# Performance work log

Hardware: AMD Instinct MI355X
Metric: run time of the kernel (lower is better)

Reference implementation:

```python
import jax, jax.numpy as jnp
import numpy as np

HIDDEN = 2048
NH = 32       # num query heads
NKV = 8       # num kv heads
D = 64        # head_dim = hidden // NH
BSX, BSY = 32, 32  # block sizes


def setup_inputs() -> dict:
    key = jax.random.key(0)
    ks = jax.random.split(key, 5)
    B, L = 2, 4096  # L = x_dim * y_dim
    w = lambda k, sh, fan: jax.random.normal(k, sh, jnp.float32) * (fan ** -0.5)
    return {
        "hidden_states": jax.random.normal(ks[0], (B, L, HIDDEN), jnp.float32),
        "Wq": w(ks[1], (HIDDEN, NH * D), HIDDEN),
        "Wk": w(ks[2], (HIDDEN, NKV * D), HIDDEN),
        "Wv": w(ks[3], (HIDDEN, NKV * D), HIDDEN),
        "Wo": w(ks[4], (NH * D, HIDDEN), NH * D),
        "x_dim": 64,
        "y_dim": 64,
    }


def _block_split(x, B, bnx, bny, h):
    # einops: 'b (bnx bsx bny bsy) (h d) -> (b bnx bny) (bsx bsy) h d'
    x = x.reshape(B, bnx, BSX, bny, BSY, h, D)
    x = x.transpose(0, 1, 3, 2, 4, 5, 6)  # b bnx bny bsx bsy h d
    return x.reshape(B * bnx * bny, BSX * BSY, h, D)


def reference(hidden_states, Wq, Wk, Wv, Wo, x_dim, y_dim):
    B, L, _ = hidden_states.shape
    bnx, bny = x_dim // BSX, y_dim // BSY
    q = _block_split(hidden_states @ Wq, B, bnx, bny, NH)   # [nb, T, NH, D]
    k = _block_split(hidden_states @ Wk, B, bnx, bny, NKV)  # [nb, T, NKV, D]
    v = _block_split(hidden_states @ Wv, B, bnx, bny, NKV)
    g = NH // NKV  # GQA groups: query head i attends kv head i // g
    k = jnp.repeat(k, g, axis=2)
    v = jnp.repeat(v, g, axis=2)
    scores = jnp.einsum('nqhd,nkhd->nhqk', q, k) * (D ** -0.5)
    p = jax.nn.softmax(scores, axis=-1)
    o = jnp.einsum('nhqk,nkhd->nqhd', p, v)  # [nb, T, NH, D]
    # Faithful to the torch code: plain reshape (does NOT invert the block rearrange)
    o = o.reshape(B, L, NH * D)
    return o @ Wo
```

## Files before the change

### kernel.cpp

```cpp
#include <hip/hip_runtime.h>

typedef __bf16 bf16_t;
typedef __bf16 bf16x8 __attribute__((ext_vector_type(8)));
typedef __bf16 bf16x4 __attribute__((ext_vector_type(4)));
typedef float f32x4 __attribute__((ext_vector_type(4)));
typedef float f32x16 __attribute__((ext_vector_type(16)));
typedef short s16x4 __attribute__((ext_vector_type(4)));
typedef short s16x8 __attribute__((ext_vector_type(8)));

#define MFMA16(A_, B_, C_) __builtin_amdgcn_mfma_f32_16x16x32_bf16((A_), (B_), (C_), 0, 0, 0)
#define MFMA32(A_, B_, C_) __builtin_amdgcn_mfma_f32_32x32x16_bf16((A_), (B_), (C_), 0, 0, 0)

#define QSC 0.18033688011112042f

__device__ __forceinline__ void gload_lds16(const bf16_t* g, bf16_t* l) {
  __builtin_amdgcn_global_load_lds(
      (const __attribute__((address_space(1))) void*)g,
      (__attribute__((address_space(3))) void*)l, 16, 0, 0);
}

__device__ __forceinline__ unsigned cvt_pk_bf16(float a, float b) {
  unsigned r;
  asm("v_cvt_pk_bf16_f32 %0, %1, %2" : "=v"(r) : "v"(a), "v"(b));
  return r;
}

__device__ __forceinline__ s16x4 tr_b16(const bf16_t* p) {
  s16x4 d;
  unsigned off = (unsigned)(size_t)(const __attribute__((address_space(3))) bf16_t*)p;
  asm volatile("ds_read_b64_tr_b16 %0, %1" : "=v"(d) : "v"(off));
  return d;
}

union B128 { s16x8 s; bf16x8 b; };

#define DSR(PTR, U)                                                           \
  do {                                                                        \
    unsigned _o = (unsigned)(size_t)                                          \
        (const __attribute__((address_space(3))) bf16_t*)(PTR);               \
    asm volatile("ds_read_b128 %0, %1" : "=v"((U).s) : "v"(_o));              \
  } while (0)

__device__ __forceinline__ void swap32(unsigned a, unsigned b, int hi,
                                       unsigned& ra, unsigned& rb) {
  unsigned bx = (unsigned)__shfl_xor((int)b, 32);
  unsigned ax = (unsigned)__shfl_xor((int)a, 32);
  ra = hi ? a : bx;
  rb = hi ? ax : b;
}

__global__ __launch_bounds__(256) void k_convert(const float* __restrict__ in,
                                                 bf16_t* __restrict__ out, int n4) {
  int i = blockIdx.x * 256 + threadIdx.x;
  if (i >= n4) return;
  float4 v = ((const float4*)in)[i];
  bf16x4 o;
  o[0] = (__bf16)v.x; o[1] = (__bf16)v.y; o[2] = (__bf16)v.z; o[3] = (__bf16)v.w;
  *(bf16x4*)(out + (size_t)i * 4) = o;
}

__global__ __launch_bounds__(256) void k_transpose(const float* __restrict__ in,
                                                   bf16_t* __restrict__ out, int R, int C) {
  __shared__ float tile[64][65];
  int tx = threadIdx.x & 63;
  int ty = threadIdx.x >> 6;
  int bc = blockIdx.x * 64;
  int br = blockIdx.y * 64;
#pragma unroll
  for (int i = ty; i < 64; i += 4)
    tile[i][tx] = in[(size_t)(br + i) * C + bc + tx];
  __syncthreads();
#pragma unroll
  for (int i = ty; i < 64; i += 4)
    out[(size_t)(bc + i) * R + br + tx] = (bf16_t)tile[tx][i];
}

__device__ __forceinline__ int permrow(int r) {
  int b  = r >> 12;
  int l  = r & 4095;
  int ix = (l >> 11) & 1;
  int sx = (l >> 6) & 31;
  int iy = (l >> 5) & 1;
  int sy = l & 31;
  return (b << 12) + (ix << 11) + (iy << 10) + (sx << 5) + sy;
}

#define LSLOT(B_, M_, H_) (lds + (((B_)*4 + (M_)*2 + (H_)) << 13))

#define STAGE_A(BUF, HF, T)                                                     \
  gload_lds16(aB + (size_t)((HF)*128) * 2048 + (T)*64, LSLOT(BUF, 0, HF) + wofs); \
  gload_lds16(aB + (size_t)((HF)*128 + 64) * 2048 + (T)*64,                     \
              LSLOT(BUF, 0, HF) + wofs + 4096);

#define STAGE_B(BUF, HF, T)                                                     \
  gload_lds16(bB + (size_t)((HF)*128) * 2048 + (T)*64, LSLOT(BUF, 1, HF) + wofs); \
  gload_lds16(bB + (size_t)((HF)*128 + 64) * 2048 + (T)*64,                     \
              LSLOT(BUF, 1, HF) + wofs + 4096);

#define LOAD_A(BUF, Q)                                                          \
  { const bf16_t* Ah = LSLOT(BUF, 0, wm) + ((Q)*32 + cl) * 64;                  \
    DSR(Ah + ((g16 * 8) ^ swz8), af[0][0]);                                     \
    DSR(Ah + ((32 + g16 * 8) ^ swz8), af[0][1]);                                \
    DSR(Ah + 1024 + ((g16 * 8) ^ swz8), af[1][0]);                              \
    DSR(Ah + 1024 + ((32 + g16 * 8) ^ swz8), af[1][1]); }

#define LOAD_B(BUF)                                                             \
  { const bf16_t* Bh = LSLOT(BUF, 1, wn >> 1);                                  \
    _Pragma("unroll") for (int ni = 0; ni < 4; ++ni) {                          \
      const bf16_t* Br = Bh + ((wn & 1) * 64 + ni * 16 + cl) * 64;              \
      DSR(Br + ((g16 * 8) ^ swz8), bfr[ni][0]);                                 \
      DSR(Br + ((32 + g16 * 8) ^ swz8), bfr[ni][1]); } }

#define MFMA_QUAD(Q)                                                            \
  _Pragma("unroll") for (int kk = 0; kk < 2; ++kk)                              \
    _Pragma("unroll") for (int ni = 0; ni < 4; ++ni) {                          \
      acc[2*(Q)][ni]   = MFMA16(af[0][kk].b, bfr[ni][kk].b, acc[2*(Q)][ni]);    \
      acc[2*(Q)+1][ni] = MFMA16(af[1][kk].b, bfr[ni][kk].b, acc[2*(Q)+1][ni]); }

#define PH_MID(VM4)                                                             \
  if (VM4) asm volatile("s_waitcnt vmcnt(4)" ::: "memory");                     \
  __builtin_amdgcn_s_barrier();                                                 \
  asm volatile("s_waitcnt lgkmcnt(0)" ::: "memory");                            \
  __builtin_amdgcn_sched_barrier(0);                                            \
  __builtin_amdgcn_s_setprio(1);

#define PH_END                                                                  \
  __builtin_amdgcn_sched_barrier(0);                                            \
  __builtin_amdgcn_s_setprio(0);                                                \
  __builtin_amdgcn_s_barrier();

template <int MODE>
__global__ __launch_bounds__(512, 2) void k_gemm8(
    const bf16_t* __restrict__ A,
    const bf16_t* __restrict__ B0, const bf16_t* __restrict__ B1,
    const bf16_t* __restrict__ B2,
    bf16_t* __restrict__ Cq, bf16_t* __restrict__ Ck, bf16_t* __restrict__ Cv,
    float* __restrict__ Cf) {
  extern __shared__ bf16_t lds[];

  int nwg = gridDim.x;
  int cpx = nwg >> 3;
  int bid = blockIdx.x;
  int swz = (bid & 7) * cpx + (bid >> 3);
  int tm = swz & 31;
  int tn = swz >> 5;

  const bf16_t* Bp;
  int brow;
  if (MODE == 0) {
    if (tn < 8)       { Bp = B0; brow = tn << 8; }
    else if (tn < 10) { Bp = B1; brow = (tn - 8) << 8; }
    else              { Bp = B2; brow = (tn - 10) << 8; }
  } else {
    Bp = B0; brow = tn << 8;
  }

  int tid = threadIdx.x;
  int lane = tid & 63;
  int w = tid >> 6;
  int wm = w >> 2, wn = w & 3;
  int g16 = lane >> 4, cl = lane & 15;
  int swz8 = (cl & 7) << 3;
  int wofs = w << 9;

  int srow = tid >> 3;
  int lc = (((tid & 7) ^ (srow & 7)) << 3);
  const bf16_t* aB = A + (size_t)(tm * 256 + srow) * 2048 + lc;
  const bf16_t* bB = Bp + (size_t)(brow + srow) * 2048 + lc;

  f32x4 acc[8][4];
#pragma unroll
  for (int i = 0; i < 8; ++i)
#pragma unroll
    for (int j = 0; j < 4; ++j) acc[i][j] = (f32x4)(0.0f);

  STAGE_A(0, 0, 0); STAGE_A(0, 1, 0);
  STAGE_B(0, 0, 0); STAGE_B(0, 1, 0);
  STAGE_B(1, 0, 1); STAGE_B(1, 1, 1);
  asm volatile("s_waitcnt vmcnt(4)" ::: "memory");
  __builtin_amdgcn_s_barrier();

  for (int it2 = 0; it2 < 16; ++it2) {
    int t1 = 2 * it2 + 1;
    int tf = 2 * it2 + 2; if (tf > 31) tf = 31;
    int tg = 2 * it2 + 3; if (tg > 31) tg = 31;
    B128 af[2][2], bfr[4][2];
    STAGE_A(1, 0, t1);
    LOAD_B(0); LOAD_A(0, 0);
    PH_MID(0); MFMA_QUAD(0); PH_END;
    STAGE_A(1, 1, t1);
    LOAD_A(0, 1);
    PH_MID(0); MFMA_QUAD(1); PH_END;
    STAGE_B(0, 0, tf);
    LOAD_A(0, 2);
    PH_MID(0); MFMA_QUAD(2); PH_END;
    STAGE_B(0, 1, tf);
    LOAD_A(0, 3);
    PH_MID(1); MFMA_QUAD(3); PH_END;
    STAGE_A(0, 0, tf);
    LOAD_B(1); LOAD_A(1, 0);
    PH_MID(0); MFMA_QUAD(0); PH_END;
    STAGE_A(0, 1, tf);
    LOAD_A(1, 1);
    PH_MID(0); MFMA_QUAD(1); PH_END;
    STAGE_B(1, 0, tg);
    LOAD_A(1, 2);
    PH_MID(0); MFMA_QUAD(2); PH_END;
    STAGE_B(1, 1, tg);
    LOAD_A(1, 3);
    PH_MID(1); MFMA_QUAD(3); PH_END;
  }

#pragma unroll
  for (int mi = 0; mi < 8; ++mi) {
#pragma unroll
    for (int rr = 0; rr < 4; ++rr) {
      int r = tm * 256 + wm * 128 + mi * 16 + g16 * 4 + rr;
      if (MODE == 0) {
        int rp = permrow(r);
#pragma unroll
        for (int ni = 0; ni < 4; ++ni) {
          int c = tn * 256 + wn * 64 + ni * 16 + cl;
          float v = acc[mi][ni][rr];
          if (c < 2048)      Cq[(size_t)rp * 2048 + c] = (bf16_t)(v * QSC);
          else if (c < 2560) Ck[(size_t)rp * 512 + (c - 2048)] = (bf16_t)v;
          else               Cv[(size_t)rp * 512 + (c - 2560)] = (bf16_t)v;
        }
      } else {
#pragma unroll
        for (int ni = 0; ni < 4; ++ni) {
          int c = tn * 256 + wn * 64 + ni * 16 + cl;
          Cf[(size_t)r * 2048 + c] = acc[mi][ni][rr];
        }
      }
    }
  }
}

__global__ __launch_bounds__(256, 2) void k_attn(
    const bf16_t* __restrict__ Qp, const bf16_t* __restrict__ Kp,
    const bf16_t* __restrict__ Vp, bf16_t* __restrict__ O) {
  int bid = blockIdx.x;
  int qc = bid & 7;
  int h  = (bid >> 3) & 31;
  int n  = bid >> 8;
  int kvh = h >> 2;

  __shared__ bf16_t buf[2][8192];

  int tid = threadIdx.x, lane = tid & 63, w = tid >> 6;
  int l31 = lane & 31, hi = lane >> 5;
  int qrow_blk = n * 1024 + qc * 128;
  bf16_t* base = &buf[0][0];

#pragma unroll
  for (int r = 0; r < 4; ++r) {
    int ql = r * 32 + (tid >> 3);
    int cs = (tid & 7) << 4;
    int lc = (cs ^ ((ql & 7) << 4)) >> 1;
    gload_lds16(Qp + (size_t)(qrow_blk + ql) * 2048 + h * 64 + lc,
                base + r * 2048 + w * 512);
  }
  __syncthreads();
  bf16x8 qf[4];
  {
    int q = w * 32 + l31;
    const bf16_t* qrow = base + q * 64;
    int sw = (q & 7) << 4;
#pragma unroll
    for (int c = 0; c < 4; ++c)
      qf[c] = *(const bf16x8*)(qrow + (((c * 32 + hi * 16) ^ sw) >> 1));
  }
  __syncthreads();

  f32x16 oacc0 = (f32x16)(0.0f), oacc1 = (f32x16)(0.0f);
  float m_run = -1e30f, l_run = 0.0f;

  auto stageKV = [&](int t) {
    bf16_t* bp = &buf[t & 1][0];
    int kvb = n * 1024 + t * 64;
#pragma unroll
    for (int r = 0; r < 2; ++r) {
      int kv = r * 32 + (tid >> 3);
      int cs = (tid & 7) << 4;
      int lc = (cs ^ ((kv & 7) << 4)) >> 1;
      gload_lds16(Kp + (size_t)(kvb + kv) * 512 + kvh * 64 + lc,
                  bp + r * 2048 + w * 512);
    }
#pragma unroll
    for (int r = 0; r < 2; ++r) {
      int slot = r * 256 + tid;
      int sub = slot >> 3;
      int kb = sub >> 2, db = sub & 3;
      int j = (slot >> 1) & 3, hf = slot & 1;
      gload_lds16(Vp + (size_t)(kvb + kb * 4 + j) * 512 + kvh * 64 + db * 16 + hf * 8,
                  bp + 4096 + r * 2048 + w * 512);
    }
  };

  stageKV(0);
  for (int t = 0; t < 16; ++t) {
    __syncthreads();
    if (t < 15) stageKV(t + 1);
    const bf16_t* bp = &buf[t & 1][0];
    const bf16_t* Vs = bp + 4096;

#pragma unroll
    for (int s = 0; s < 2; ++s) {
      f32x16 st = (f32x16)(0.0f);
      {
        int kv = s * 32 + l31;
        const bf16_t* krow = bp + kv * 64;
        int sw = (kv & 7) << 4;
#pragma unroll
        for (int c = 0; c < 4; ++c) {
          bf16x8 kf = *(const bf16x8*)(krow + (((c * 32 + hi * 16) ^ sw) >> 1));
          st = MFMA32(kf, qf[c], st);
        }
      }
      float a0 = fmaxf(st[0], st[1]),   a1 = fmaxf(st[2], st[3]);
      float a2 = fmaxf(st[4], st[5]),   a3 = fmaxf(st[6], st[7]);
      float a4 = fmaxf(st[8], st[9]),   a5 = fmaxf(st[10], st[11]);
      float a6 = fmaxf(st[12], st[13]), a7 = fmaxf(st[14], st[15]);
      float pmax = fmaxf(fmaxf(fmaxf(a0, a1), fmaxf(a2, a3)),
                         fmaxf(fmaxf(a4, a5), fmaxf(a6, a7)));
      pmax = fmaxf(pmax, __shfl_xor(pmax, 32));
      if (!__all(pmax <= m_run + 11.0f)) {
        float mnew = fmaxf(m_run, pmax);
        float resc = exp2f(m_run - mnew);
        l_run *= resc;
#pragma unroll
        for (int e = 0; e < 16; ++e) { oacc0[e] *= resc; oacc1[e] *= resc; }
        m_run = mnew;
      }
      float rs = 0.0f;
      unsigned pw[8];
#pragma unroll
      for (int u = 0; u < 8; ++u) {
        float p0 = exp2f(st[2 * u] - m_run);
        float p1 = exp2f(st[2 * u + 1] - m_run);
        rs += p0 + p1;
        pw[u] = cvt_pk_bf16(p0, p1);
      }
      rs += __shfl_xor(rs, 32);
      l_run += rs;

#pragma unroll
      for (int c = 0; c < 2; ++c) {
        unsigned w2, w0, w3, w1;
        swap32(pw[c * 4 + 2], pw[c * 4 + 0], hi, w2, w0);
        swap32(pw[c * 4 + 3], pw[c * 4 + 1], hi, w3, w1);
        union { unsigned u[4]; bf16x8 v; } pa;
        pa.u[0] = w0; pa.u[1] = w1; pa.u[2] = w2; pa.u[3] = w3;
        int kb0 = s * 8 + c * 4 + hi * 2;
        int dbl = l31 >> 4;
        int cc8 = (l31 & 15) * 4;
        const bf16_t* p00 = Vs + (kb0 * 4 + dbl) * 64 + cc8;
        const bf16_t* p01 = Vs + ((kb0 + 1) * 4 + dbl) * 64 + cc8;
        const bf16_t* p10 = Vs + (kb0 * 4 + 2 + dbl) * 64 + cc8;
        const bf16_t* p11 = Vs + ((kb0 + 1) * 4 + 2 + dbl) * 64 + cc8;
        s16x4 t00 = tr_b16(p00), t01 = tr_b16(p01);
        s16x4 t10 = tr_b16(p10), t11 = tr_b16(p11);
        asm volatile("s_waitcnt lgkmcnt(0)" ::: "memory");
        __builtin_amdgcn_sched_barrier(0);
        union { s16x4 s4[2]; bf16x8 v; } vf0, vf1;
        vf0.s4[0] = t00; vf0.s4[1] = t01;
        vf1.s4[0] = t10; vf1.s4[1] = t11;
        oacc0 = MFMA32(pa.v, vf0.v, oacc0);
        oacc1 = MFMA32(pa.v, vf1.v, oacc1);
      }
    }
  }

  float linv = 1.0f / l_run;
#pragma unroll
  for (int r = 0; r < 16; ++r) {
    int qrw = (r & 3) + 8 * (r >> 2) + 4 * hi;
    float li = __shfl(linv, qrw);
    size_t orow = (size_t)(qrow_blk + w * 32 + qrw) * 2048 + h * 64 + l31;
    O[orow]      = (bf16_t)(oacc0[r] * li);
    O[orow + 32] = (bf16_t)(oacc1[r] * li);
  }
}

extern "C" void kernel_launch(void* const* d_in, const int* in_sizes, int n_in,
                              void* d_out, int out_size, void* d_ws, size_t ws_size,
                              hipStream_t stream) {
  const float* X  = (const float*)d_in[0];
  const float* Wq = (const float*)d_in[1];
  const float* Wk = (const float*)d_in[2];
  const float* Wv = (const float*)d_in[3];
  const float* Wo = (const float*)d_in[4];
  float* out = (float*)d_out;

  char* ws = (char*)d_ws;
  const size_t MB = 1024 * 1024;
  bf16_t* Xb  = (bf16_t*)(ws + 0);
  bf16_t* WqT = (bf16_t*)(ws + 32 * MB);
  bf16_t* WkT = (bf16_t*)(ws + 40 * MB);
  bf16_t* WvT = (bf16_t*)(ws + 42 * MB);
  bf16_t* WoT = (bf16_t*)(ws + 44 * MB);
  bf16_t* Qp  = (bf16_t*)(ws + 52 * MB);
  bf16_t* Kp  = (bf16_t*)(ws + 84 * MB);
  bf16_t* Vp  = (bf16_t*)(ws + 92 * MB);
  bf16_t* Ob  = (bf16_t*)(ws + 100 * MB);

  hipFuncSetAttribute(reinterpret_cast<const void*>(&k_gemm8<0>),
                      hipFuncAttributeMaxDynamicSharedMemorySize, 131072);
  hipFuncSetAttribute(reinterpret_cast<const void*>(&k_gemm8<1>),
                      hipFuncAttributeMaxDynamicSharedMemorySize, 131072);

  k_convert<<<16384, 256, 0, stream>>>(X, Xb, 4194304);
  k_transpose<<<dim3(32, 32), 256, 0, stream>>>(Wq, WqT, 2048, 2048);
  k_transpose<<<dim3(8, 32), 256, 0, stream>>>(Wk, WkT, 2048, 512);
  k_transpose<<<dim3(8, 32), 256, 0, stream>>>(Wv, WvT, 2048, 512);
  k_transpose<<<dim3(32, 32), 256, 0, stream>>>(Wo, WoT, 2048, 2048);

  k_gemm8<0><<<384, 512, 131072, stream>>>(Xb, WqT, WkT, WvT, Qp, Kp, Vp, nullptr);
  k_attn<<<2048, 256, 0, stream>>>(Qp, Kp, Vp, Ob);
  k_gemm8<1><<<256, 512, 131072, stream>>>(Ob, WoT, nullptr, nullptr, nullptr,
                                           nullptr, nullptr, out);
}
```

Measured before the change: 354.2 us.

## Merge GEMM pipeline phases into fewer, larger MFMA blocks and retile block swizzle

Restructures the 8-phase-per-iteration GEMM main loop into 4 phases. Each phase now loads four A fragments and issues 32 MFMAs instead of 16, which halves the number of barriers and priority switches per K-step. The workgroup-to-tile mapping is also changed so each XCD-group of blocks covers 4 consecutive M-tiles across all N-tiles, to improve L2 reuse. The cost is higher register pressure from the larger fragment arrays and coarser overlap between global staging and compute.

```diff
diff --git a/kernel.cpp b/kernel.cpp
--- a/kernel.cpp
+++ b/kernel.cpp
@@ -97,12 +97,11 @@
   gload_lds16(bB + (size_t)((HF)*128 + 64) * 2048 + (T)*64,                     \
               LSLOT(BUF, 1, HF) + wofs + 4096);
 
-#define LOAD_A(BUF, Q)                                                          \
-  { const bf16_t* Ah = LSLOT(BUF, 0, wm) + ((Q)*32 + cl) * 64;                  \
-    DSR(Ah + ((g16 * 8) ^ swz8), af[0][0]);                                     \
-    DSR(Ah + ((32 + g16 * 8) ^ swz8), af[0][1]);                                \
-    DSR(Ah + 1024 + ((g16 * 8) ^ swz8), af[1][0]);                              \
-    DSR(Ah + 1024 + ((32 + g16 * 8) ^ swz8), af[1][1]); }
+#define LOAD_A2(BUF, H)                                                         \
+  { const bf16_t* Ah = LSLOT(BUF, 0, wm) + ((H)*64 + cl) * 64;                  \
+    _Pragma("unroll") for (int j = 0; j < 4; ++j) {                             \
+      DSR(Ah + j * 1024 + ((g16 * 8) ^ swz8), af[j][0]);                        \
+      DSR(Ah + j * 1024 + ((32 + g16 * 8) ^ swz8), af[j][1]); } }
 
 #define LOAD_B(BUF)                                                             \
   { const bf16_t* Bh = LSLOT(BUF, 1, wn >> 1);                                  \
@@ -111,11 +110,12 @@
       DSR(Br + ((g16 * 8) ^ swz8), bfr[ni][0]);                                 \
       DSR(Br + ((32 + g16 * 8) ^ swz8), bfr[ni][1]); } }
 
-#define MFMA_QUAD(Q)                                                            \
+#define MFMA_OCT(H)                                                             \
   _Pragma("unroll") for (int kk = 0; kk < 2; ++kk)                              \
-    _Pragma("unroll") for (int ni = 0; ni < 4; ++ni) {                          \
-      acc[2*(Q)][ni]   = MFMA16(af[0][kk].b, bfr[ni][kk].b, acc[2*(Q)][ni]);    \
-      acc[2*(Q)+1][ni] = MFMA16(af[1][kk].b, bfr[ni][kk].b, acc[2*(Q)+1][ni]); }
+    _Pragma("unroll") for (int j = 0; j < 4; ++j)                               \
+      _Pragma("unroll") for (int ni = 0; ni < 4; ++ni)                          \
+        acc[(H)*4 + j][ni] =                                                    \
+            MFMA16(af[j][kk].b, bfr[ni][kk].b, acc[(H)*4 + j][ni]);
 
 #define PH_MID(VM4)                                                             \
   if (VM4) asm volatile("s_waitcnt vmcnt(4)" ::: "memory");                     \
@@ -138,12 +138,11 @@
     float* __restrict__ Cf) {
   extern __shared__ bf16_t lds[];
 
-  int nwg = gridDim.x;
-  int cpx = nwg >> 3;
+  const int TN = (MODE == 0) ? 12 : 8;
   int bid = blockIdx.x;
-  int swz = (bid & 7) * cpx + (bid >> 3);
-  int tm = swz & 31;
-  int tn = swz >> 5;
+  int s = bid >> 3;
+  int tm = (bid & 7) * 4 + s / TN;
+  int tn = s % TN;
 
   const bf16_t* Bp;
   int brow;
@@ -184,31 +183,19 @@
     int t1 = 2 * it2 + 1;
     int tf = 2 * it2 + 2; if (tf > 31) tf = 31;
     int tg = 2 * it2 + 3; if (tg > 31) tg = 31;
-    B128 af[2][2], bfr[4][2];
-    STAGE_A(1, 0, t1);
-    LOAD_B(0); LOAD_A(0, 0);
-    PH_MID(0); MFMA_QUAD(0); PH_END;
-    STAGE_A(1, 1, t1);
-    LOAD_A(0, 1);
-    PH_MID(0); MFMA_QUAD(1); PH_END;
-    STAGE_B(0, 0, tf);
-    LOAD_A(0, 2);
-    PH_MID(0); MFMA_QUAD(2); PH_END;
-    STAGE_B(0, 1, tf);
-    LOAD_A(0, 3);
-    PH_MID(1); MFMA_QUAD(3); PH_END;
-    STAGE_A(0, 0, tf);
-    LOAD_B(1); LOAD_A(1, 0);
-    PH_MID(0); MFMA_QUAD(0); PH_END;
-    STAGE_A(0, 1, tf);
-    LOAD_A(1, 1);
-    PH_MID(0); MFMA_QUAD(1); PH_END;
-    STAGE_B(1, 0, tg);
-    LOAD_A(1, 2);
-    PH_MID(0); MFMA_QUAD(2); PH_END;
-    STAGE_B(1, 1, tg);
-    LOAD_A(1, 3);
-    PH_MID(1); MFMA_QUAD(3); PH_END;
+    B128 af[4][2], bfr[4][2];
+    STAGE_A(1, 0, t1); STAGE_A(1, 1, t1);
+    LOAD_B(0); LOAD_A2(0, 0);
+    PH_MID(0); MFMA_OCT(0); PH_END;
+    STAGE_B(0, 0, tf); STAGE_B(0, 1, tf);
+    LOAD_A2(0, 1);
+    PH_MID(1); MFMA_OCT(1); PH_END;
+    STAGE_A(0, 0, tf); STAGE_A(0, 1, tf);
+    LOAD_B(1); LOAD_A2(1, 0);
+    PH_MID(0); MFMA_OCT(0); PH_END;
+    STAGE_B(1, 0, tg); STAGE_B(1, 1, tg);
+    LOAD_A2(1, 1);
+    PH_MID(1); MFMA_OCT(1); PH_END;
   }
 
 #pragma unroll
```

After: 354.7 us. No clear change (+0.1%).

## Use 256x128 tiles with triple-buffered LDS pipeline for QKV projection GEMM

Applied to the files above, without the earlier changes.

Replaces the templated 256x256-tile GEMM for the fused QKV projection with a dedicated kernel using 256x128 tiles, 768 workgroups, and a three-slot LDS ring buffer that stages two k-steps ahead. This raises the workgroup count so the 256 CUs are filled more evenly (384 large tiles leave a partial second wave). It also changes the block-to-tile mapping to a fixed XCD-aware swizzle for both GEMMs. The cost is lower arithmetic intensity per tile, so more global traffic for the shared operand, and 144KB of LDS per workgroup, which limits each CU to one resident workgroup.

```diff
diff --git a/kernel.cpp b/kernel.cpp
--- a/kernel.cpp
+++ b/kernel.cpp
@@ -85,6 +85,128 @@
   return (b << 12) + (ix << 11) + (iy << 10) + (sx << 5) + sy;
 }
 
+#define SBAR __builtin_amdgcn_sched_barrier(0)
+
+#define LA(K_) (lds + (K_)*24576)
+#define LB(K_) (lds + (K_)*24576 + 16384)
+
+__global__ __launch_bounds__(512, 2) void k_gemmA(
+    const bf16_t* __restrict__ A,
+    const bf16_t* __restrict__ B0, const bf16_t* __restrict__ B1,
+    const bf16_t* __restrict__ B2,
+    bf16_t* __restrict__ Cq, bf16_t* __restrict__ Ck, bf16_t* __restrict__ Cv) {
+  extern __shared__ bf16_t lds[];
+
+  int bid = blockIdx.x;
+  int s = bid >> 3;
+  int tm = (bid & 7) * 4 + s / 24;
+  int tn = s % 24;
+
+  const bf16_t* Bp;
+  int brow;
+  if (tn < 16)      { Bp = B0; brow = tn << 7; }
+  else if (tn < 20) { Bp = B1; brow = (tn - 16) << 7; }
+  else              { Bp = B2; brow = (tn - 20) << 7; }
+
+  int tid = threadIdx.x;
+  int lane = tid & 63;
+  int w = tid >> 6;
+  int wm = w >> 1, wn = w & 1;
+  int g16 = lane >> 4, cl = lane & 15;
+  int swz8 = (cl & 7) << 3;
+  int wofs = w << 9;
+
+  int srow = tid >> 3;
+  int lc = (((tid & 7) ^ (srow & 7)) << 3);
+  const bf16_t* aB = A + (size_t)(tm * 256 + srow) * 2048 + lc;
+  const bf16_t* bB = Bp + (size_t)(brow + srow) * 2048 + lc;
+
+#define GA_STAGE_A(K_, T_)                                                     \
+  _Pragma("unroll") for (int rr = 0; rr < 4; ++rr)                             \
+    gload_lds16(aB + (size_t)(rr * 64) * 2048 + (T_)*64,                       \
+                LA(K_) + rr * 4096 + wofs);
+
+#define GA_STAGE_B(K_, T_)                                                     \
+  _Pragma("unroll") for (int rr = 0; rr < 2; ++rr)                             \
+    gload_lds16(bB + (size_t)(rr * 64) * 2048 + (T_)*64,                       \
+                LB(K_) + rr * 4096 + wofs);
+
+#define GA_RD_B(K_)                                                            \
+  _Pragma("unroll") for (int ni = 0; ni < 4; ++ni) {                           \
+    const bf16_t* Br = LB(K_) + (wn * 64 + ni * 16 + cl) * 64;                 \
+    DSR(Br + ((g16 * 8) ^ swz8), bfr[ni][0]);                                  \
+    DSR(Br + ((32 + g16 * 8) ^ swz8), bfr[ni][1]);                             \
+  }
+
+#define GA_RD_A(K_, MB_)                                                       \
+  _Pragma("unroll") for (int m = 0; m < 2; ++m) {                              \
+    const bf16_t* Ar = LA(K_) + (wm * 64 + ((MB_) + m) * 16 + cl) * 64;        \
+    DSR(Ar + ((g16 * 8) ^ swz8), af[m][0]);                                    \
+    DSR(Ar + ((32 + g16 * 8) ^ swz8), af[m][1]);                               \
+  }
+
+#define GA_MFMA(MB_)                                                           \
+  _Pragma("unroll") for (int kk = 0; kk < 2; ++kk)                             \
+    _Pragma("unroll") for (int m = 0; m < 2; ++m)                              \
+      _Pragma("unroll") for (int ni = 0; ni < 4; ++ni)                         \
+        acc[(MB_) + m][ni] =                                                   \
+            MFMA16(af[m][kk].b, bfr[ni][kk].b, acc[(MB_) + m][ni]);
+
+#define GA_MID                                                                 \
+  __builtin_amdgcn_s_barrier();                                                \
+  asm volatile("s_waitcnt lgkmcnt(0)" ::: "memory");                           \
+  SBAR;                                                                        \
+  __builtin_amdgcn_s_setprio(1);
+
+#define GA_END                                                                 \
+  SBAR;                                                                        \
+  __builtin_amdgcn_s_setprio(0);                                               \
+  __builtin_amdgcn_s_barrier();
+
+  f32x4 acc[4][4];
+#pragma unroll
+  for (int i = 0; i < 4; ++i)
+#pragma unroll
+    for (int j = 0; j < 4; ++j) acc[i][j] = (f32x4)(0.0f);
+
+  GA_STAGE_A(0, 0); GA_STAGE_B(0, 0);
+  GA_STAGE_A(1, 1); GA_STAGE_B(1, 1);
+  asm volatile("s_waitcnt vmcnt(6)" ::: "memory");
+  __builtin_amdgcn_s_barrier();
+
+  int k = 0;
+  for (int t = 0; t < 32; ++t) {
+    int k2 = k + 2; if (k2 >= 3) k2 -= 3;
+    int t2 = t + 2; if (t2 > 31) t2 = 31;
+    B128 af[2][2], bfr[4][2];
+    GA_RD_B(k); GA_RD_A(k, 0);
+    GA_STAGE_A(k2, t2);
+    GA_MID; GA_MFMA(0); GA_END;
+    GA_RD_A(k, 2);
+    asm volatile("s_waitcnt vmcnt(4)" ::: "memory");
+    GA_STAGE_B(k2, t2);
+    GA_MID; GA_MFMA(2); GA_END;
+    ++k; if (k == 3) k = 0;
+  }
+
+#pragma unroll
+  for (int mi = 0; mi < 4; ++mi) {
+#pragma unroll
+    for (int rr = 0; rr < 4; ++rr) {
+      int r = tm * 256 + wm * 64 + mi * 16 + g16 * 4 + rr;
+      int rp = permrow(r);
+#pragma unroll
+      for (int ni = 0; ni < 4; ++ni) {
+        int c = tn * 128 + wn * 64 + ni * 16 + cl;
+        float v = acc[mi][ni][rr];
+        if (c < 2048)      Cq[(size_t)rp * 2048 + c] = (bf16_t)(v * QSC);
+        else if (c < 2560) Ck[(size_t)rp * 512 + (c - 2048)] = (bf16_t)v;
+        else               Cv[(size_t)rp * 512 + (c - 2560)] = (bf16_t)v;
+      }
+    }
+  }
+}
+
 #define LSLOT(B_, M_, H_) (lds + (((B_)*4 + (M_)*2 + (H_)) << 13))
 
 #define STAGE_A(BUF, HF, T)                                                     \
@@ -121,39 +243,25 @@
   if (VM4) asm volatile("s_waitcnt vmcnt(4)" ::: "memory");                     \
   __builtin_amdgcn_s_barrier();                                                 \
   asm volatile("s_waitcnt lgkmcnt(0)" ::: "memory");                            \
-  __builtin_amdgcn_sched_barrier(0);                                            \
+  SBAR;                                                                         \
   __builtin_amdgcn_s_setprio(1);
 
 #define PH_END                                                                  \
-  __builtin_amdgcn_sched_barrier(0);                                            \
+  SBAR;                                                                         \
   __builtin_amdgcn_s_setprio(0);                                                \
   __builtin_amdgcn_s_barrier();
 
-template <int MODE>
-__global__ __launch_bounds__(512, 2) void k_gemm8(
-    const bf16_t* __restrict__ A,
-    const bf16_t* __restrict__ B0, const bf16_t* __restrict__ B1,
-    const bf16_t* __restrict__ B2,
-    bf16_t* __restrict__ Cq, bf16_t* __restrict__ Ck, bf16_t* __restrict__ Cv,
+__global__ __launch_bounds__(512, 2) void k_gemmB(
+    const bf16_t* __restrict__ A, const bf16_t* __restrict__ B0,
     float* __restrict__ Cf) {
   extern __shared__ bf16_t lds[];
 
-  int nwg = gridDim.x;
-  int cpx = nwg >> 3;
   int bid = blockIdx.x;
-  int swz = (bid & 7) * cpx + (bid >> 3);
-  int tm = swz & 31;
-  int tn = swz >> 5;
-
-  const bf16_t* Bp;
-  int brow;
-  if (MODE == 0) {
-    if (tn < 8)       { Bp = B0; brow = tn << 8; }
-    else if (tn < 10) { Bp = B1; brow = (tn - 8) << 8; }
-    else              { Bp = B2; brow = (tn - 10) << 8; }
-  } else {
-    Bp = B0; brow = tn << 8;
-  }
+  int s = bid >> 3;
+  int tm = (bid & 7) * 4 + (s >> 3);
+  int tn = s & 7;
+  const bf16_t* Bp = B0;
+  int brow = tn << 8;
 
   int tid = threadIdx.x;
   int lane = tid & 63;
@@ -216,22 +324,10 @@
 #pragma unroll
     for (int rr = 0; rr < 4; ++rr) {
       int r = tm * 256 + wm * 128 + mi * 16 + g16 * 4 + rr;
-      if (MODE == 0) {
-        int rp = permrow(r);
-#pragma unroll
-        for (int ni = 0; ni < 4; ++ni) {
-          int c = tn * 256 + wn * 64 + ni * 16 + cl;
-          float v = acc[mi][ni][rr];
-          if (c < 2048)      Cq[(size_t)rp * 2048 + c] = (bf16_t)(v * QSC);
-          else if (c < 2560) Ck[(size_t)rp * 512 + (c - 2048)] = (bf16_t)v;
-          else               Cv[(size_t)rp * 512 + (c - 2560)] = (bf16_t)v;
-        }
-      } else {
-#pragma unroll
-        for (int ni = 0; ni < 4; ++ni) {
-          int c = tn * 256 + wn * 64 + ni * 16 + cl;
-          Cf[(size_t)r * 2048 + c] = acc[mi][ni][rr];
-        }
+#pragma unroll
+      for (int ni = 0; ni < 4; ++ni) {
+        int c = tn * 256 + wn * 64 + ni * 16 + cl;
+        Cf[(size_t)r * 2048 + c] = acc[mi][ni][rr];
       }
     }
   }
@@ -405,9 +501,9 @@
   bf16_t* Vp  = (bf16_t*)(ws + 92 * MB);
   bf16_t* Ob  = (bf16_t*)(ws + 100 * MB);
 
-  hipFuncSetAttribute(reinterpret_cast<const void*>(&k_gemm8<0>),
-                      hipFuncAttributeMaxDynamicSharedMemorySize, 131072);
-  hipFuncSetAttribute(reinterpret_cast<const void*>(&k_gemm8<1>),
+  hipFuncSetAttribute(reinterpret_cast<const void*>(&k_gemmA),
+                      hipFuncAttributeMaxDynamicSharedMemorySize, 147456);
+  hipFuncSetAttribute(reinterpret_cast<const void*>(&k_gemmB),
                       hipFuncAttributeMaxDynamicSharedMemorySize, 131072);
 
   k_convert<<<16384, 256, 0, stream>>>(X, Xb, 4194304);
@@ -416,8 +512,7 @@
   k_transpose<<<dim3(8, 32), 256, 0, stream>>>(Wv, WvT, 2048, 512);
   k_transpose<<<dim3(32, 32), 256, 0, stream>>>(Wo, WoT, 2048, 2048);
 
-  k_gemm8<0><<<384, 512, 131072, stream>>>(Xb, WqT, WkT, WvT, Qp, Kp, Vp, nullptr);
+  k_gemmA<<<768, 512, 147456, stream>>>(Xb, WqT, WkT, WvT, Qp, Kp, Vp);
   k_attn<<<2048, 256, 0, stream>>>(Qp, Kp, Vp, Ob);
-  k_gemm8<1><<<256, 512, 131072, stream>>>(Ob, WoT, nullptr, nullptr, nullptr,
-                                           nullptr, nullptr, out);
-}
+  k_gemmB<<<256, 512, 131072, stream>>>(Ob, WoT, out);
+}
```

Measured after the change: 353.9 us. No clear change (-0.1%).
